# Kernel tuning notes

Hardware: AMD Instinct MI355X
Metric: run time of the kernel (lower is better)

The kernel has to match this reference:

```python
import jax, jax.numpy as jnp
import numpy as np

B, T, D, H, C = 256, 512, 128, 512, 10

def setup_inputs() -> dict:
    key = jax.random.key(0)
    ks = jax.random.split(key, 12)
    s_x = 1.0 / np.sqrt(D)
    s_h = 1.0 / np.sqrt(H)
    inp = {
        'x':   jax.random.normal(ks[0], (B, T, D), dtype=jnp.float32),
        'wgx': jax.random.normal(ks[1], (D, H), dtype=jnp.float32) * s_x,
        'wgh': jax.random.normal(ks[2], (H, H), dtype=jnp.float32) * s_h,
        'bg':  jnp.zeros((H,), dtype=jnp.float32),
        'wix': jax.random.normal(ks[3], (D, H), dtype=jnp.float32) * s_x,
        'wih': jax.random.normal(ks[4], (H, H), dtype=jnp.float32) * s_h,
        'bi':  jnp.zeros((H,), dtype=jnp.float32),
        'wfx': jax.random.normal(ks[5], (D, H), dtype=jnp.float32) * s_x,
        'wfh': jax.random.normal(ks[6], (H, H), dtype=jnp.float32) * s_h,
        'bf':  jnp.ones((H,), dtype=jnp.float32),  # forget bias = 1 as in source
        'wox': jax.random.normal(ks[7], (D, H), dtype=jnp.float32) * s_x,
        'woh': jax.random.normal(ks[8], (H, H), dtype=jnp.float32) * s_h,
        'bo':  jnp.zeros((H,), dtype=jnp.float32),
        'wph': jax.random.normal(ks[9], (H, C), dtype=jnp.float32) * s_h,
        'bp':  jnp.zeros((C,), dtype=jnp.float32),
    }
    return inp

def reference(x, wgx, wgh, bg, wix, wih, bi, wfx, wfh, bf, wox, woh, bo, wph, bp):
    # Precompute all input projections as one big batched GEMM per gate: [B,T,H]
    xg = jnp.einsum('btd,dh->bth', x, wgx) + bg
    xi = jnp.einsum('btd,dh->bth', x, wix) + bi
    xf = jnp.einsum('btd,dh->bth', x, wfx) + bf
    xo = jnp.einsum('btd,dh->bth', x, wox) + bo

    def step(carry, xt):
        h_prev, c_prev = carry
        xg_t, xi_t, xf_t, xo_t = xt
        gt = jnp.tanh(xg_t + h_prev @ wgh)
        it = jax.nn.sigmoid(xi_t + h_prev @ wih)
        ft = jax.nn.sigmoid(xf_t + h_prev @ wfh)
        ot = jax.nn.sigmoid(xo_t + h_prev @ woh)
        ct = gt * it + c_prev * ft
        ht = jnp.tanh(ct) * ot
        return (ht, ct), None

    h0 = jnp.zeros((x.shape[0], wgh.shape[0]), dtype=x.dtype)
    c0 = jnp.zeros_like(h0)
    # scan over time: move T to leading axis
    xs = (xg.swapaxes(0, 1), xi.swapaxes(0, 1), xf.swapaxes(0, 1), xo.swapaxes(0, 1))
    (hT, _), _ = jax.lax.scan(step, (h0, c0), xs)
    return hT @ wph + bp
```

## Files before the change

kernel.cpp:

```cpp
#include <hip/hip_runtime.h>
#include <hip/hip_bf16.h>
#include <stdint.h>

typedef __attribute__((ext_vector_type(8))) short short8;
typedef __attribute__((ext_vector_type(4))) float floatx4;
typedef __attribute__((ext_vector_type(4))) int intx4;
typedef __attribute__((ext_vector_type(2))) unsigned long long ull2;
typedef __attribute__((ext_vector_type(4))) unsigned short ushort4v;

#define DEVI __device__ __forceinline__

constexpr int B_ = 256, T_ = 512, D_ = 128, H_ = 512, C_ = 10;
constexpr int KTOT = H_ + D_;
constexpr int RG = 16;
constexpr int NBG = 16;
constexpr int NCG = 16;
constexpr int HCW = 32;

constexpr size_t OFF_XB = 0;
constexpr size_t SZ_XB  = (size_t)B_ * T_ * D_ * 2;
constexpr size_t OFF_WC = OFF_XB + SZ_XB;
constexpr size_t SZ_WC  = (size_t)4 * H_ * KTOT * 2;
constexpr size_t OFF_HB = OFF_WC + SZ_WC;
constexpr size_t SZ_HB  = (size_t)2 * B_ * H_ * 2;
constexpr size_t OFF_CT = OFF_HB + SZ_HB;
constexpr size_t SZ_CT  = (size_t)NBG * (T_ + 1) * 4;
constexpr size_t WS_NEED = OFF_CT + SZ_CT;

DEVI uint16_t f2bf(float f) {
    uint32_t u = __builtin_bit_cast(uint32_t, f);
    u += 0x7FFFu + ((u >> 16) & 1u);
    return (uint16_t)(u >> 16);
}
DEVI float bf2f(uint16_t u) {
    return __builtin_bit_cast(float, (uint32_t)u << 16);
}
DEVI float sigf(float x)  { return 1.0f / (1.0f + __expf(-x)); }
DEVI float tanhf_(float x){ return 1.0f - 2.0f / (1.0f + __expf(2.0f * x)); }

__global__ void k_cvt_x(const float* __restrict__ x, uint16_t* __restrict__ xb) {
    int i = (blockIdx.x * 256 + threadIdx.x) * 4;
    float4 v = *reinterpret_cast<const float4*>(x + i);
    ushort4v o;
    o.x = f2bf(v.x); o.y = f2bf(v.y); o.z = f2bf(v.z); o.w = f2bf(v.w);
    *reinterpret_cast<ushort4v*>(xb + i) = o;
}

__global__ void k_build_w(const float* __restrict__ wgh, const float* __restrict__ wih,
                          const float* __restrict__ wfh, const float* __restrict__ woh,
                          const float* __restrict__ wgx, const float* __restrict__ wix,
                          const float* __restrict__ wfx, const float* __restrict__ wox,
                          uint16_t* __restrict__ wc) {
    int np = blockIdx.x;
    int g = np >> 9, n = np & 511;
    const float* wh = (g == 0) ? wgh : (g == 1) ? wih : (g == 2) ? wfh : woh;
    const float* wx = (g == 0) ? wgx : (g == 1) ? wix : (g == 2) ? wfx : wox;
    for (int k = threadIdx.x; k < KTOT; k += 256) {
        float v = (k < H_) ? wh[(size_t)k * H_ + n] : wx[(size_t)(k - H_) * H_ + n];
        wc[(size_t)np * KTOT + k] = f2bf(v);
    }
}

#define WLOAD(dst, base, IMM) \
    asm volatile("global_load_dwordx4 %0, %1, off offset:" #IMM \
                 : "=v"(dst) : "v"(base))
#define WLOAD20(arr, base) \
    WLOAD(arr[0],  base, 0);    WLOAD(arr[1],  base, 64);   \
    WLOAD(arr[2],  base, 128);  WLOAD(arr[3],  base, 192);  \
    WLOAD(arr[4],  base, 256);  WLOAD(arr[5],  base, 320);  \
    WLOAD(arr[6],  base, 384);  WLOAD(arr[7],  base, 448);  \
    WLOAD(arr[8],  base, 512);  WLOAD(arr[9],  base, 576);  \
    WLOAD(arr[10], base, 640);  WLOAD(arr[11], base, 704);  \
    WLOAD(arr[12], base, 768);  WLOAD(arr[13], base, 832);  \
    WLOAD(arr[14], base, 896);  WLOAD(arr[15], base, 960);  \
    WLOAD(arr[16], base, 1024); WLOAD(arr[17], base, 1088); \
    WLOAD(arr[18], base, 1152); WLOAD(arr[19], base, 1216)

__global__ __launch_bounds__(256, 1) void k_lstm(
    const uint16_t* __restrict__ xb,
    const uint16_t* __restrict__ wc,
    const float* __restrict__ bgp, const float* __restrict__ bip,
    const float* __restrict__ bfp, const float* __restrict__ bop,
    uint16_t* hbuf,
    int* counters)
{
    __shared__ __align__(16) short hx[RG * KTOT];
    __shared__ float pre[4][RG][HCW + 1];

    const int tid  = threadIdx.x;
    const int lane = tid & 63;
    const int w    = tid >> 6;
    const int bid  = blockIdx.x;
    const int xcd = bid & 7, j = bid >> 3;
    const int bg = xcd * 2 + (j >> 4);
    const int cg = j & 15;
    const int b0  = bg * RG;
    const int hc0 = cg * HCW;

    short8 bfr0[20], bfr1[20];
    {
        const int lcol = lane & 15, kgrp = lane >> 4;
        const uint16_t* src0 = wc + (size_t)(w * H_ + hc0 + 0  + lcol) * KTOT + kgrp * 8;
        const uint16_t* src1 = wc + (size_t)(w * H_ + hc0 + 16 + lcol) * KTOT + kgrp * 8;
        WLOAD20(bfr0, src0);
        WLOAD20(bfr1, src1);
        asm volatile("s_waitcnt vmcnt(0)" ::: "memory");
    }

    const int erow = tid >> 4;
    const int ep   = tid & 15;
    const int hcg0 = hc0 + ep * 2;
    float bge[2], bie[2], bfe[2], boe[2], cst[2] = {0.f, 0.f};
    #pragma unroll
    for (int e = 0; e < 2; ++e) {
        bge[e] = bgp[hcg0 + e]; bie[e] = bip[hcg0 + e];
        bfe[e] = bfp[hcg0 + e]; boe[e] = bop[hcg0 + e];
    }

    const int srow = tid >> 4, sseg = tid & 15;
    const int sswz = (srow & 7) << 4;
    const int arow = lane & 15, akg = lane >> 4;
    const int abase = arow * (KTOT * 2) + akg * 16;
    const int aswz  = (arow & 7) << 4;
    const int hrow0 = (lane >> 4) * 4;

    int* ctr = counters + bg * (T_ + 1);
    char* lds = (char*)hx;

    for (int t = 0; t < T_; ++t) {
        {
            const short8 xv = *reinterpret_cast<const short8*>(
                xb + ((size_t)(b0 + srow) * T_ + t) * D_ + sseg * 8);
            int byte = srow * (KTOT * 2) + H_ * 2 + sseg * 16;
            *reinterpret_cast<short8*>(lds + (byte ^ sswz)) = xv;
        }

        if (t > 0) {
            if (tid == 0) {
                int it = 0;
                while (__hip_atomic_load(ctr + t, __ATOMIC_RELAXED, __HIP_MEMORY_SCOPE_AGENT) < NCG) {
                    if (++it > (1 << 28)) break;
                    __builtin_amdgcn_s_sleep(1);
                }
                asm volatile("" ::: "memory");
            }
            __syncthreads();
        }

        if (t == 0) {
            intx4 z = {0, 0, 0, 0};
            #pragma unroll
            for (int c4 = 0; c4 < 4; ++c4) {
                int byte = srow * (KTOT * 2) + sseg * 64 + c4 * 16;
                *reinterpret_cast<intx4*>(lds + (byte ^ sswz)) = z;
            }
        } else {
            const unsigned long long* src = reinterpret_cast<const unsigned long long*>(
                hbuf + (size_t)(t & 1) * B_ * H_ + (size_t)(b0 + srow) * H_ + sseg * 32);
            #pragma unroll
            for (int c4 = 0; c4 < 4; ++c4) {
                unsigned long long lov = __hip_atomic_load(src + c4 * 2,     __ATOMIC_RELAXED, __HIP_MEMORY_SCOPE_AGENT);
                unsigned long long hiv = __hip_atomic_load(src + c4 * 2 + 1, __ATOMIC_RELAXED, __HIP_MEMORY_SCOPE_AGENT);
                ull2 v; v.x = lov; v.y = hiv;
                int byte = srow * (KTOT * 2) + sseg * 64 + c4 * 16;
                *reinterpret_cast<ull2*>(lds + (byte ^ sswz)) = v;
            }
        }
        __syncthreads();

        floatx4 acc0 = {0.f, 0.f, 0.f, 0.f}, acc1 = {0.f, 0.f, 0.f, 0.f};
        #pragma unroll
        for (int ks = 0; ks < 20; ++ks) {
            int byte = (abase + ks * 64) ^ aswz;
            short8 a = *reinterpret_cast<const short8*>(lds + byte);
            acc0 = __builtin_amdgcn_mfma_f32_16x16x32_bf16(a, bfr0[ks], acc0, 0, 0, 0);
            acc1 = __builtin_amdgcn_mfma_f32_16x16x32_bf16(a, bfr1[ks], acc1, 0, 0, 0);
        }
        #pragma unroll
        for (int r = 0; r < 4; ++r) {
            pre[w][(lane >> 4) * 4 + r][(lane & 15)]      = acc0[r];
            pre[w][(lane >> 4) * 4 + r][16 + (lane & 15)] = acc1[r];
        }
        __syncthreads();

        float hp[2];
        #pragma unroll
        for (int e = 0; e < 2; ++e) {
            int col = ep * 2 + e;
            float ag = pre[0][erow][col] + bge[e];
            float ai = pre[1][erow][col] + bie[e];
            float af = pre[2][erow][col] + bfe[e];
            float ao = pre[3][erow][col] + boe[e];
            float g = tanhf_(ag), ii = sigf(ai), f = sigf(af), o = sigf(ao);
            float c = g * ii + cst[e] * f;
            cst[e] = c;
            hp[e] = tanhf_(c) * o;
        }
        uint32_t packed = (uint32_t)f2bf(hp[0]) | ((uint32_t)f2bf(hp[1]) << 16);
        uint32_t* hdst = reinterpret_cast<uint32_t*>(
            hbuf + (size_t)((t + 1) & 1) * B_ * H_ + (size_t)(b0 + erow) * H_ + hcg0);
        __hip_atomic_store(hdst, packed, __ATOMIC_RELAXED, __HIP_MEMORY_SCOPE_AGENT);
        asm volatile("s_waitcnt vmcnt(0)" ::: "memory");
        __syncthreads();
        if (tid == 0)
            __hip_atomic_fetch_add(ctr + t + 1, 1, __ATOMIC_RELAXED, __HIP_MEMORY_SCOPE_AGENT);
    }
}

__global__ void k_proj(const uint16_t* __restrict__ hb0, const float* __restrict__ wph,
                       const float* __restrict__ bp, float* __restrict__ out) {
    int b = blockIdx.x, lane = threadIdx.x;
    const uint32_t* hrow = reinterpret_cast<const uint32_t*>(hb0 + (size_t)b * H_);
    float p[C_];
    #pragma unroll
    for (int c = 0; c < C_; ++c) p[c] = 0.f;
    #pragma unroll
    for (int q = 0; q < 4; ++q) {
        int k2 = lane + q * 64;
        uint32_t u = __hip_atomic_load(hrow + k2, __ATOMIC_RELAXED, __HIP_MEMORY_SCOPE_AGENT);
        float h0 = bf2f((uint16_t)(u & 0xFFFFu));
        float h1 = bf2f((uint16_t)(u >> 16));
        #pragma unroll
        for (int c = 0; c < C_; ++c)
            p[c] += h0 * wph[(size_t)(2 * k2) * C_ + c] + h1 * wph[(size_t)(2 * k2 + 1) * C_ + c];
    }
    #pragma unroll
    for (int c = 0; c < C_; ++c) {
        float v = p[c];
        #pragma unroll
        for (int off = 32; off; off >>= 1) v += __shfl_down(v, off, 64);
        if (lane == 0) out[(size_t)b * C_ + c] = v + bp[c];
    }
}

extern "C" void kernel_launch(void* const* d_in, const int* in_sizes, int n_in,
                              void* d_out, int out_size, void* d_ws, size_t ws_size,
                              hipStream_t stream) {
    const float* x   = (const float*)d_in[0];
    const float* wgx = (const float*)d_in[1];
    const float* wgh = (const float*)d_in[2];
    const float* bg  = (const float*)d_in[3];
    const float* wix = (const float*)d_in[4];
    const float* wih = (const float*)d_in[5];
    const float* bi  = (const float*)d_in[6];
    const float* wfx = (const float*)d_in[7];
    const float* wfh = (const float*)d_in[8];
    const float* bf  = (const float*)d_in[9];
    const float* wox = (const float*)d_in[10];
    const float* woh = (const float*)d_in[11];
    const float* bo  = (const float*)d_in[12];
    const float* wph = (const float*)d_in[13];
    const float* bp  = (const float*)d_in[14];

    if (ws_size < WS_NEED) return;

    char* ws = (char*)d_ws;
    uint16_t* xbp = (uint16_t*)(ws + OFF_XB);
    uint16_t* wcp = (uint16_t*)(ws + OFF_WC);
    uint16_t* hbp = (uint16_t*)(ws + OFF_HB);
    int*      ctp = (int*)(ws + OFF_CT);

    hipMemsetAsync(ctp, 0, SZ_CT, stream);
    k_cvt_x<<<(B_ * T_ * D_) / (256 * 4), 256, 0, stream>>>(x, xbp);
    k_build_w<<<4 * H_, 256, 0, stream>>>(wgh, wih, wfh, woh, wgx, wix, wfx, wox, wcp);
    k_lstm<<<256, 256, 0, stream>>>(xbp, wcp, bg, bi, bf, bo, hbp, ctp);
    k_proj<<<B_, 64, 0, stream>>>(hbp , wph, bp, (float*)d_out);
}
```

Measured before the change: 1.620 ms.

## Replace per-step atomic counters with per-producer flags and coherent vector h loads

```diff
diff --git a/kernel.cpp b/kernel.cpp
--- a/kernel.cpp
+++ b/kernel.cpp
@@ -5,7 +5,7 @@
 typedef __attribute__((ext_vector_type(8))) short short8;
 typedef __attribute__((ext_vector_type(4))) float floatx4;
 typedef __attribute__((ext_vector_type(4))) int intx4;
-typedef __attribute__((ext_vector_type(2))) unsigned long long ull2;
+typedef __attribute__((ext_vector_type(4))) unsigned int uintx4;
 typedef __attribute__((ext_vector_type(4))) unsigned short ushort4v;
 
 #define DEVI __device__ __forceinline__
@@ -23,9 +23,9 @@
 constexpr size_t SZ_WC  = (size_t)4 * H_ * KTOT * 2;
 constexpr size_t OFF_HB = OFF_WC + SZ_WC;
 constexpr size_t SZ_HB  = (size_t)2 * B_ * H_ * 2;
-constexpr size_t OFF_CT = OFF_HB + SZ_HB;
-constexpr size_t SZ_CT  = (size_t)NBG * (T_ + 1) * 4;
-constexpr size_t WS_NEED = OFF_CT + SZ_CT;
+constexpr size_t OFF_FL = OFF_HB + SZ_HB;
+constexpr size_t SZ_FL  = (size_t)NBG * NCG * 64;
+constexpr size_t WS_NEED = OFF_FL + SZ_FL;
 
 DEVI uint16_t f2bf(float f) {
     uint32_t u = __builtin_bit_cast(uint32_t, f);
@@ -76,16 +76,20 @@
     WLOAD(arr[16], base, 1024); WLOAD(arr[17], base, 1088); \
     WLOAD(arr[18], base, 1152); WLOAD(arr[19], base, 1216)
 
+#define HLOAD(dst, base, IMM) \
+    asm volatile("global_load_dwordx4 %0, %1, off offset:" #IMM " sc0 sc1" \
+                 : "=v"(dst) : "v"(base) : "memory")
+
 __global__ __launch_bounds__(256, 1) void k_lstm(
     const uint16_t* __restrict__ xb,
     const uint16_t* __restrict__ wc,
     const float* __restrict__ bgp, const float* __restrict__ bip,
     const float* __restrict__ bfp, const float* __restrict__ bop,
     uint16_t* hbuf,
-    int* counters)
+    int* flags)
 {
     __shared__ __align__(16) short hx[RG * KTOT];
-    __shared__ float pre[4][RG][HCW + 1];
+    __shared__ float pre[4][RG][HCW + 2];
 
     const int tid  = threadIdx.x;
     const int lane = tid & 63;
@@ -108,8 +112,8 @@
     }
 
     const int erow = tid >> 4;
-    const int ep   = tid & 15;
-    const int hcg0 = hc0 + ep * 2;
+    const int epr  = tid & 15;
+    const int hcg0 = hc0 + epr * 2;
     float bge[2], bie[2], bfe[2], boe[2], cst[2] = {0.f, 0.f};
     #pragma unroll
     for (int e = 0; e < 2; ++e) {
@@ -122,9 +126,8 @@
     const int arow = lane & 15, akg = lane >> 4;
     const int abase = arow * (KTOT * 2) + akg * 16;
     const int aswz  = (arow & 7) << 4;
-    const int hrow0 = (lane >> 4) * 4;
-
-    int* ctr = counters + bg * (T_ + 1);
+
+    int* fbase = flags + bg * NCG * 16;
     char* lds = (char*)hx;
 
     for (int t = 0; t < T_; ++t) {
@@ -136,10 +139,15 @@
         }
 
         if (t > 0) {
-            if (tid == 0) {
+            if (w == 0) {
                 int it = 0;
-                while (__hip_atomic_load(ctr + t, __ATOMIC_RELAXED, __HIP_MEMORY_SCOPE_AGENT) < NCG) {
-                    if (++it > (1 << 28)) break;
+                for (;;) {
+                    int f = t;
+                    if (lane < NCG)
+                        f = __hip_atomic_load(fbase + lane * 16, __ATOMIC_RELAXED,
+                                              __HIP_MEMORY_SCOPE_AGENT);
+                    if (__ballot(f == t) == ~0ull) break;
+                    if (++it > (1 << 22)) break;
                     __builtin_amdgcn_s_sleep(1);
                 }
                 asm volatile("" ::: "memory");
@@ -155,15 +163,17 @@
                 *reinterpret_cast<intx4*>(lds + (byte ^ sswz)) = z;
             }
         } else {
-            const unsigned long long* src = reinterpret_cast<const unsigned long long*>(
+            const uint32_t* src = reinterpret_cast<const uint32_t*>(
                 hbuf + (size_t)(t & 1) * B_ * H_ + (size_t)(b0 + srow) * H_ + sseg * 32);
+            uintx4 v0, v1, v2, v3;
+            HLOAD(v0, src, 0);  HLOAD(v1, src, 16);
+            HLOAD(v2, src, 32); HLOAD(v3, src, 48);
+            asm volatile("s_waitcnt vmcnt(0)" ::: "memory");
             #pragma unroll
             for (int c4 = 0; c4 < 4; ++c4) {
-                unsigned long long lov = __hip_atomic_load(src + c4 * 2,     __ATOMIC_RELAXED, __HIP_MEMORY_SCOPE_AGENT);
-                unsigned long long hiv = __hip_atomic_load(src + c4 * 2 + 1, __ATOMIC_RELAXED, __HIP_MEMORY_SCOPE_AGENT);
-                ull2 v; v.x = lov; v.y = hiv;
+                uintx4 v = (c4 == 0) ? v0 : (c4 == 1) ? v1 : (c4 == 2) ? v2 : v3;
                 int byte = srow * (KTOT * 2) + sseg * 64 + c4 * 16;
-                *reinterpret_cast<ull2*>(lds + (byte ^ sswz)) = v;
+                *reinterpret_cast<uintx4*>(lds + (byte ^ sswz)) = v;
             }
         }
         __syncthreads();
@@ -186,7 +196,7 @@
         float hp[2];
         #pragma unroll
         for (int e = 0; e < 2; ++e) {
-            int col = ep * 2 + e;
+            int col = epr * 2 + e;
             float ag = pre[0][erow][col] + bge[e];
             float ai = pre[1][erow][col] + bie[e];
             float af = pre[2][erow][col] + bfe[e];
@@ -203,7 +213,8 @@
         asm volatile("s_waitcnt vmcnt(0)" ::: "memory");
         __syncthreads();
         if (tid == 0)
-            __hip_atomic_fetch_add(ctr + t + 1, 1, __ATOMIC_RELAXED, __HIP_MEMORY_SCOPE_AGENT);
+            __hip_atomic_store(fbase + cg * 16, t + 1, __ATOMIC_RELAXED,
+                               __HIP_MEMORY_SCOPE_AGENT);
     }
 }
 
@@ -258,11 +269,11 @@
     uint16_t* xbp = (uint16_t*)(ws + OFF_XB);
     uint16_t* wcp = (uint16_t*)(ws + OFF_WC);
     uint16_t* hbp = (uint16_t*)(ws + OFF_HB);
-    int*      ctp = (int*)(ws + OFF_CT);
-
-    hipMemsetAsync(ctp, 0, SZ_CT, stream);
+    int*      flp = (int*)(ws + OFF_FL);
+
+    hipMemsetAsync(flp, 0, SZ_FL, stream);
     k_cvt_x<<<(B_ * T_ * D_) / (256 * 4), 256, 0, stream>>>(x, xbp);
     k_build_w<<<4 * H_, 256, 0, stream>>>(wgh, wih, wfh, woh, wgx, wix, wfx, wox, wcp);
-    k_lstm<<<256, 256, 0, stream>>>(xbp, wcp, bg, bi, bf, bo, hbp, ctp);
+    k_lstm<<<256, 256, 0, stream>>>(xbp, wcp, bg, bi, bf, bo, hbp, flp);
     k_proj<<<B_, 64, 0, stream>>>(hbp , wph, bp, (float*)d_out);
 }
```

Result: faster. 1.345 ms (-17.0%).
